# Optimization experiments

Hardware: AMD Instinct MI355X
Metric: run time of the kernel (lower is better)

The kernel has to match this reference:

```python
import jax, jax.numpy as jnp
import numpy as np

N_NODES = 20000
N_EDGES = 160000
N_GRAPHS = 64
IN_DIM = 128
HID = 512
N_ACT = 32


def gcn_conv(x, W, b, src, dst, n_nodes):
    # PyG GCNConv: add self-loops, symmetric normalization, x @ W then scatter-add.
    loop = jnp.arange(n_nodes, dtype=src.dtype)
    s = jnp.concatenate([src, loop])
    d = jnp.concatenate([dst, loop])
    deg = jax.ops.segment_sum(jnp.ones_like(d, dtype=x.dtype), d, num_segments=n_nodes)
    dinv = jnp.where(deg > 0, jax.lax.rsqrt(deg), 0.0)
    norm = dinv[s] * dinv[d]                      # [E+N]
    h = x @ W                                     # [N, out]
    msg = h[s] * norm[:, None]                    # gather + scale
    out = jax.ops.segment_sum(msg, d, num_segments=n_nodes)
    return out + b


def setup_inputs() -> dict:
    key = jax.random.key(0)
    ks = jax.random.split(key, 16)
    tree_x = jax.random.normal(ks[0], (N_NODES, IN_DIM), dtype=jnp.float32)
    edge_index = jax.random.randint(ks[1], (2, N_EDGES), 0, N_NODES, dtype=jnp.int32)
    # batch assignment: guarantee every graph id appears, then sort
    raw = jnp.concatenate([jnp.arange(N_GRAPHS, dtype=jnp.int32),
                           jax.random.randint(ks[2], (N_NODES - N_GRAPHS,), 0, N_GRAPHS, dtype=jnp.int32)])
    batch = jnp.sort(raw)

    def glorot(k, shape):
        lim = np.sqrt(6.0 / (shape[0] + shape[1]))
        return jax.random.uniform(k, shape, jnp.float32, -lim, lim)

    params = {
        'W1': glorot(ks[3], (IN_DIM, HID)), 'b1': jnp.zeros((HID,), jnp.float32),
        'W2': glorot(ks[4], (HID, HID)),    'b2': jnp.zeros((HID,), jnp.float32),
        'W3': glorot(ks[5], (HID, HID)),    'b3': jnp.zeros((HID,), jnp.float32),
        'Wf1': glorot(ks[6], (HID, HID)),   'bf1': jnp.zeros((HID,), jnp.float32),
        'Wf2': glorot(ks[7], (HID, HID)),   'bf2': jnp.zeros((HID,), jnp.float32),
        'Wf3': glorot(ks[8], (HID, HID)),   'bf3': jnp.zeros((HID,), jnp.float32),
        'Wo': glorot(ks[9], (HID, N_ACT)),  'bo': jnp.zeros((N_ACT,), jnp.float32),
    }
    return {'tree_x': tree_x, 'edge_index': edge_index, 'batch': batch, **params}


def reference(tree_x, edge_index, batch, W1, b1, W2, b2, W3, b3,
              Wf1, bf1, Wf2, bf2, Wf3, bf3, Wo, bo):
    src, dst = edge_index[0], edge_index[1]
    h = jax.nn.relu(gcn_conv(tree_x, W1, b1, src, dst, N_NODES))
    h = jax.nn.relu(gcn_conv(h, W2, b2, src, dst, N_NODES))
    h = jax.nn.relu(gcn_conv(h, W3, b3, src, dst, N_NODES))
    x = jax.ops.segment_max(h, batch, num_segments=N_GRAPHS)  # global_max_pool
    x = jax.nn.relu(x @ Wf1 + bf1)
    x = jax.nn.relu(x @ Wf2 + bf2)
    x = jax.nn.relu(x @ Wf3 + bf3)
    return x @ Wo + bo
```

## Files before the change

kernel.cpp:

```cpp
#include <hip/hip_runtime.h>
#include <stdint.h>

#define N_NODES 20000
#define N_EDGES 160000
#define N_GRAPHS 64
#define IN_DIM 128
#define HID 512
#define N_ACT 32

#define SCAN_NB ((N_NODES + 255) / 256)

typedef __attribute__((ext_vector_type(8))) short short8;
typedef __attribute__((ext_vector_type(4))) float f32x4;

__device__ __forceinline__ float bf2f(uint h16) {
    union { uint u; float f; } v; v.u = h16 << 16; return v.f;
}
__device__ __forceinline__ float bflo(uint u) {
    union { uint x; float f; } v; v.x = u << 16; return v.f;
}
__device__ __forceinline__ float bfhi(uint u) {
    union { uint x; float f; } v; v.x = u & 0xffff0000u; return v.f;
}
__device__ __forceinline__ ushort f2bf(float f) {
    union { float f; uint u; } v; v.f = f;
    uint u = v.u;
    uint r = (u + 0x7fffu + ((u >> 16) & 1u)) >> 16;
    return (ushort)r;
}

__device__ __forceinline__ void add8(float* acc, uint4 v) {
    acc[0] += bflo(v.x); acc[1] += bfhi(v.x);
    acc[2] += bflo(v.y); acc[3] += bfhi(v.y);
    acc[4] += bflo(v.z); acc[5] += bfhi(v.z);
    acc[6] += bflo(v.w); acc[7] += bfhi(v.w);
}


#define PB_HIST   625
#define PB_F2BF   (PB_HIST + 10000)
#define PB_WT1    (PB_F2BF + 64)
#define PB_WT2    (PB_WT1 + 256)
#define PB_WT3    (PB_WT2 + 256)
#define PB_BOUNDS (PB_WT3 + SCAN_NB)

__global__ __launch_bounds__(256) void k_prep(
    const int* __restrict__ edst, int* __restrict__ cnt,
    const float* __restrict__ tree_x, ushort* __restrict__ xbf,
    const float* __restrict__ W1, ushort* __restrict__ w1t,
    const float* __restrict__ W2, ushort* __restrict__ w2t,
    const float* __restrict__ W3, ushort* __restrict__ w3t,
    const int* __restrict__ batch, int* __restrict__ gstart)
{
    __shared__ float lds[32][33];
    int b = blockIdx.x;
    int t = threadIdx.x;
    int r = t >> 5, c = t & 31;
    if (b < PB_HIST) {
        int e = b * 256 + t;
        if (e < N_EDGES) atomicAdd(&cnt[edst[e]], 1);
    } else if (b < PB_F2BF) {
        int i = (b - PB_HIST) * 256 + t;
        if (i < N_NODES * IN_DIM) xbf[i] = f2bf(tree_x[i]);
    } else if (b < PB_WT1) {
        int tt = b - PB_F2BF;
        int kt = tt & 3, nt = tt >> 2;
        for (int rr = r; rr < 32; rr += 8)
            lds[rr][c] = W1[(size_t)(kt * 32 + rr) * HID + nt * 32 + c];
        __syncthreads();
        for (int rr = r; rr < 32; rr += 8)
            w1t[(size_t)(nt * 32 + rr) * IN_DIM + kt * 32 + c] = f2bf(lds[c][rr]);
    } else if (b < PB_WT2) {
        int tt = b - PB_WT1;
        int kt = tt & 15, nt = tt >> 4;
        for (int rr = r; rr < 32; rr += 8)
            lds[rr][c] = W2[(size_t)(kt * 32 + rr) * HID + nt * 32 + c];
        __syncthreads();
        for (int rr = r; rr < 32; rr += 8)
            w2t[(size_t)(nt * 32 + rr) * HID + kt * 32 + c] = f2bf(lds[c][rr]);
    } else if (b < PB_WT3) {
        int tt = b - PB_WT2;
        int kt = tt & 15, nt = tt >> 4;
        for (int rr = r; rr < 32; rr += 8)
            lds[rr][c] = W3[(size_t)(kt * 32 + rr) * HID + nt * 32 + c];
        __syncthreads();
        for (int rr = r; rr < 32; rr += 8)
            w3t[(size_t)(nt * 32 + rr) * HID + kt * 32 + c] = f2bf(lds[c][rr]);
    } else {
        int i = (b - PB_WT3) * 256 + t;
        if (i < N_NODES) {
            if (i == 0) {
                gstart[batch[0]] = 0;
                gstart[N_GRAPHS] = N_NODES;
            } else if (batch[i] != batch[i - 1]) {
                gstart[batch[i]] = i;
            }
        }
    }
}


__global__ __launch_bounds__(256) void k_part(const int* __restrict__ cnt, int* __restrict__ bsum) {
    __shared__ int s[256];
    int idx = blockIdx.x * 256 + threadIdx.x;
    s[threadIdx.x] = (idx < N_NODES) ? cnt[idx] : 0;
    __syncthreads();
    for (int off = 128; off > 0; off >>= 1) {
        if (threadIdx.x < off) s[threadIdx.x] += s[threadIdx.x + off];
        __syncthreads();
    }
    if (threadIdx.x == 0) bsum[blockIdx.x] = s[0];
}

__global__ __launch_bounds__(128) void k_scanb(const int* __restrict__ bsum,
                                               int* __restrict__ boff, int* __restrict__ rowstart) {
    __shared__ int s[128];
    int t = threadIdx.x;
    int own = (t < SCAN_NB) ? bsum[t] : 0;
    s[t] = own;
    __syncthreads();
    for (int off = 1; off < 128; off <<= 1) {
        int v = 0;
        if (t >= off) v = s[t - off];
        __syncthreads();
        s[t] += v;
        __syncthreads();
    }
    if (t < SCAN_NB) boff[t] = s[t] - own;
    if (t == SCAN_NB - 1) rowstart[N_NODES] = s[t];
}

__global__ __launch_bounds__(256) void k_final(
    const int* __restrict__ cnt, const int* __restrict__ boff,
    int* __restrict__ rowstart, int* __restrict__ cursor, float* __restrict__ dinv)
{
    __shared__ int s[256];
    int t = threadIdx.x;
    int idx = blockIdx.x * 256 + t;
    int c = (idx < N_NODES) ? cnt[idx] : 0;
    s[t] = c;
    __syncthreads();
    for (int off = 1; off < 256; off <<= 1) {
        int v = 0;
        if (t >= off) v = s[t - off];
        __syncthreads();
        s[t] += v;
        __syncthreads();
    }
    if (idx < N_NODES) {
        int start = boff[blockIdx.x] + s[t] - c;
        rowstart[idx] = start;
        cursor[idx] = start;
        dinv[idx] = rsqrtf((float)c + 1.0f);
    }
}

__global__ void k_fill(const int* __restrict__ src, const int* __restrict__ dst,
                       int* __restrict__ cursor, int* __restrict__ csr_src) {
    int e = blockIdx.x * 256 + threadIdx.x;
    if (e < N_EDGES) {
        int p = atomicAdd(&cursor[dst[e]], 1);
        csr_src[p] = src[e];
    }
}


__global__ __launch_bounds__(256) void k_gemm(
    const ushort* __restrict__ A, const ushort* __restrict__ Bt,
    const float* __restrict__ dinv, const float* __restrict__ bias,
    ushort* __restrict__ Out, int M, int Kdim, int mode)
{
    const int N = HID;
    __shared__ __align__(16) ushort lA[128 * 64];
    __shared__ __align__(16) ushort lB[128 * 64];
    int bm = blockIdx.x, bn = blockIdx.y;
    int tid = threadIdx.x;
    int wave = tid >> 6, lane = tid & 63;
    int wm = (wave >> 1) * 64, wn = (wave & 1) * 64;

    f32x4 acc[4][4] = {};

    int srow = lane >> 3;
    int scol = (lane & 7) * 8;

    for (int kt = 0; kt < Kdim; kt += 64) {
        for (int c = wave * 4; c < wave * 4 + 4; ++c) {
            int row = c * 8 + srow;
            int ga = bm * 128 + row; if (ga >= M) ga = M - 1;
            const ushort* gsA = A + (size_t)ga * Kdim + kt + scol;
            __builtin_amdgcn_global_load_lds(
                (const __attribute__((address_space(1))) void*)gsA,
                (__attribute__((address_space(3))) void*)(lA + c * 512), 16, 0, 0);
            int gb = bn * 128 + row;
            const ushort* gsB = Bt + (size_t)gb * Kdim + kt + scol;
            __builtin_amdgcn_global_load_lds(
                (const __attribute__((address_space(1))) void*)gsB,
                (__attribute__((address_space(3))) void*)(lB + c * 512), 16, 0, 0);
        }
        __syncthreads();
        for (int kk = 0; kk < 2; ++kk) {
            short8 af[4], bfr[4];
            int ko = kk * 32 + (lane >> 4) * 8;
            for (int m = 0; m < 4; ++m)
                af[m] = *(const short8*)&lA[(wm + m * 16 + (lane & 15)) * 64 + ko];
            for (int n = 0; n < 4; ++n)
                bfr[n] = *(const short8*)&lB[(wn + n * 16 + (lane & 15)) * 64 + ko];
            for (int m = 0; m < 4; ++m)
                for (int n = 0; n < 4; ++n)
                    acc[m][n] = __builtin_amdgcn_mfma_f32_16x16x32_bf16(af[m], bfr[n], acc[m][n], 0, 0, 0);
        }
        __syncthreads();
    }

    int cb = bn * 128 + wn + (lane & 15);
    float bb[4];
    if (mode == 1) {
        for (int n = 0; n < 4; ++n) bb[n] = bias[cb + n * 16];
    }
    for (int m = 0; m < 4; ++m) {
        int rbase = bm * 128 + wm + m * 16 + (lane >> 4) * 4;
        for (int j = 0; j < 4; ++j) {
            int r = rbase + j;
            if (r < M) {
                if (mode == 0) {
                    float dv = dinv[r];
                    for (int n = 0; n < 4; ++n)
                        Out[(size_t)r * N + cb + n * 16] = f2bf(acc[m][n][j] * dv);
                } else {
                    for (int n = 0; n < 4; ++n)
                        Out[(size_t)r * N + cb + n * 16] = f2bf(fmaxf(acc[m][n][j] + bb[n], 0.0f));
                }
            }
        }
    }
}


__global__ __launch_bounds__(256) void k_agg1(
    const ushort* __restrict__ Xin, const int* __restrict__ rowstart,
    const int* __restrict__ csr_src, const float* __restrict__ dinv,
    ushort* __restrict__ Y)
{
    int i = blockIdx.x * 4 + (threadIdx.x >> 6);
    if (i >= N_NODES) return;
    int lane = threadIdx.x & 63;
    const uint* xin = (const uint*)Xin;
    float dv = dinv[i];
    uint xi = xin[(size_t)i * 64 + lane];
    float a0 = dv * bflo(xi), a1 = dv * bfhi(xi);
    int e = rowstart[i], s1 = rowstart[i + 1];
    for (; e + 4 <= s1; e += 4) {
        int sa = csr_src[e], sb = csr_src[e + 1], sc = csr_src[e + 2], sd = csr_src[e + 3];
        float da = dinv[sa], db = dinv[sb], dc = dinv[sc], dd = dinv[sd];
        uint wa = xin[(size_t)sa * 64 + lane];
        uint wb = xin[(size_t)sb * 64 + lane];
        uint wc = xin[(size_t)sc * 64 + lane];
        uint wd = xin[(size_t)sd * 64 + lane];
        a0 = fmaf(da, bflo(wa), a0); a1 = fmaf(da, bfhi(wa), a1);
        a0 = fmaf(db, bflo(wb), a0); a1 = fmaf(db, bfhi(wb), a1);
        a0 = fmaf(dc, bflo(wc), a0); a1 = fmaf(dc, bfhi(wc), a1);
        a0 = fmaf(dd, bflo(wd), a0); a1 = fmaf(dd, bfhi(wd), a1);
    }
    for (; e < s1; ++e) {
        int sa = csr_src[e];
        float da = dinv[sa];
        uint wa = xin[(size_t)sa * 64 + lane];
        a0 = fmaf(da, bflo(wa), a0); a1 = fmaf(da, bfhi(wa), a1);
    }
    uint o = (uint)f2bf(dv * a0) | ((uint)f2bf(dv * a1) << 16);
    ((uint*)Y)[(size_t)i * 64 + lane] = o;
}


__global__ __launch_bounds__(256) void k_agg(
    const ushort* __restrict__ G, const int* __restrict__ rowstart,
    const int* __restrict__ csr_src, const float* __restrict__ dinv,
    const float* __restrict__ bias, ushort* __restrict__ X)
{
    int i = blockIdx.x * 4 + (threadIdx.x >> 6);
    if (i >= N_NODES) return;
    int lane = threadIdx.x & 63;
    const uint4* g4 = (const uint4*)G;

    uint4 a = g4[(size_t)i * 64 + lane];
    float acc[8] = { bflo(a.x), bfhi(a.x), bflo(a.y), bfhi(a.y),
                     bflo(a.z), bfhi(a.z), bflo(a.w), bfhi(a.w) };

    int e = rowstart[i], s1 = rowstart[i + 1];
    for (; e + 8 <= s1; e += 8) {
        int s0 = csr_src[e],     s1i = csr_src[e + 1], s2 = csr_src[e + 2], s3 = csr_src[e + 3];
        int s4 = csr_src[e + 4], s5 = csr_src[e + 5],  s6 = csr_src[e + 6], s7 = csr_src[e + 7];
        uint4 w0 = g4[(size_t)s0 * 64 + lane];
        uint4 w1 = g4[(size_t)s1i * 64 + lane];
        uint4 w2 = g4[(size_t)s2 * 64 + lane];
        uint4 w3 = g4[(size_t)s3 * 64 + lane];
        uint4 w4 = g4[(size_t)s4 * 64 + lane];
        uint4 w5 = g4[(size_t)s5 * 64 + lane];
        uint4 w6 = g4[(size_t)s6 * 64 + lane];
        uint4 w7 = g4[(size_t)s7 * 64 + lane];
        add8(acc, w0); add8(acc, w1); add8(acc, w2); add8(acc, w3);
        add8(acc, w4); add8(acc, w5); add8(acc, w6); add8(acc, w7);
    }
    for (; e + 4 <= s1; e += 4) {
        int s0 = csr_src[e], s1i = csr_src[e + 1], s2 = csr_src[e + 2], s3 = csr_src[e + 3];
        uint4 w0 = g4[(size_t)s0 * 64 + lane];
        uint4 w1 = g4[(size_t)s1i * 64 + lane];
        uint4 w2 = g4[(size_t)s2 * 64 + lane];
        uint4 w3 = g4[(size_t)s3 * 64 + lane];
        add8(acc, w0); add8(acc, w1); add8(acc, w2); add8(acc, w3);
    }
    for (; e < s1; ++e) {
        int s0 = csr_src[e];
        uint4 w0 = g4[(size_t)s0 * 64 + lane];
        add8(acc, w0);
    }

    float dv = dinv[i];
    float4 b0 = *(const float4*)(bias + lane * 8);
    float4 b1 = *(const float4*)(bias + lane * 8 + 4);
    float bb[8] = { b0.x, b0.y, b0.z, b0.w, b1.x, b1.y, b1.z, b1.w };

    uint4 o;
    uint p[8];
    for (int j = 0; j < 8; ++j)
        p[j] = f2bf(fmaxf(fmaf(dv, acc[j], bb[j]), 0.0f));
    o.x = p[0] | (p[1] << 16);
    o.y = p[2] | (p[3] << 16);
    o.z = p[4] | (p[5] << 16);
    o.w = p[6] | (p[7] << 16);
    *(uint4*)(X + (size_t)i * HID + lane * 8) = o;
}


__global__ __launch_bounds__(64) void k_pool(
    const ushort* __restrict__ X, const int* __restrict__ gstart, float* __restrict__ P)
{
    int g = blockIdx.x;
    int ch = blockIdx.y * 64 + threadIdx.x;
    float mx = -1e30f;
    int i0 = gstart[g], i1 = gstart[g + 1];
    int i = i0;
    for (; i + 4 <= i1; i += 4) {
        float a = bf2f(X[(size_t)(i + 0) * HID + ch]);
        float b = bf2f(X[(size_t)(i + 1) * HID + ch]);
        float c = bf2f(X[(size_t)(i + 2) * HID + ch]);
        float d = bf2f(X[(size_t)(i + 3) * HID + ch]);
        mx = fmaxf(mx, fmaxf(fmaxf(a, b), fmaxf(c, d)));
    }
    for (; i < i1; ++i) mx = fmaxf(mx, bf2f(X[(size_t)i * HID + ch]));
    P[(size_t)g * HID + ch] = mx;
}


__global__ __launch_bounds__(256) void k_fc(
    const float* __restrict__ in, const float* __restrict__ W,
    const float* __restrict__ b, float* __restrict__ out,
    int K, int NO, int relu)
{
    __shared__ float xs[HID];
    __shared__ float part[4][64];
    int g = blockIdx.x;
    int j0 = blockIdx.y * 64;
    int tid = threadIdx.x;
    int wave = tid >> 6, lane = tid & 63;

    for (int k = tid; k < K; k += 256) xs[k] = in[(size_t)g * K + k];
    __syncthreads();

    int j = j0 + lane;
    bool active = (j < NO);
    int kpw = K >> 2;
    int k0 = wave * kpw;
    float acc = 0.0f;
    if (active) {
        const float* wp = W + (size_t)k0 * NO + j;
        int k = 0;
        for (; k + 4 <= kpw; k += 4) {
            float w0 = wp[(size_t)(k + 0) * NO];
            float w1 = wp[(size_t)(k + 1) * NO];
            float w2 = wp[(size_t)(k + 2) * NO];
            float w3 = wp[(size_t)(k + 3) * NO];
            acc = fmaf(xs[k0 + k + 0], w0, acc);
            acc = fmaf(xs[k0 + k + 1], w1, acc);
            acc = fmaf(xs[k0 + k + 2], w2, acc);
            acc = fmaf(xs[k0 + k + 3], w3, acc);
        }
        for (; k < kpw; ++k)
            acc = fmaf(xs[k0 + k], wp[(size_t)k * NO], acc);
    }
    part[wave][lane] = acc;
    __syncthreads();
    if (wave == 0 && active) {
        float a = part[0][lane] + part[1][lane] + part[2][lane] + part[3][lane] + b[j];
        if (relu) a = fmaxf(a, 0.0f);
        out[(size_t)g * NO + j] = a;
    }
}


extern "C" void kernel_launch(void* const* d_in, const int* in_sizes, int n_in,
                              void* d_out, int out_size, void* d_ws, size_t ws_size,
                              hipStream_t stream) {
    const float* tree_x = (const float*)d_in[0];
    const int*   ei     = (const int*)d_in[1];
    const int*   batch  = (const int*)d_in[2];
    const float* W1  = (const float*)d_in[3];  const float* b1  = (const float*)d_in[4];
    const float* W2  = (const float*)d_in[5];  const float* b2  = (const float*)d_in[6];
    const float* W3  = (const float*)d_in[7];  const float* b3  = (const float*)d_in[8];
    const float* Wf1 = (const float*)d_in[9];  const float* bf1 = (const float*)d_in[10];
    const float* Wf2 = (const float*)d_in[11]; const float* bf2 = (const float*)d_in[12];
    const float* Wf3 = (const float*)d_in[13]; const float* bf3 = (const float*)d_in[14];
    const float* Wo  = (const float*)d_in[15]; const float* bo  = (const float*)d_in[16];

    char* w = (char*)d_ws;
    size_t off = 0;
    auto alloc = [&](size_t bytes) -> void* {
        void* p = w + off;
        off += (bytes + 255) & ~(size_t)255;
        return p;
    };
    int*    cnt      = (int*)alloc((size_t)N_NODES * 4);
    int*    cursor   = (int*)alloc((size_t)N_NODES * 4);
    int*    rowstart = (int*)alloc((size_t)(N_NODES + 1) * 4);
    float*  dinv     = (float*)alloc((size_t)N_NODES * 4);
    int*    csr      = (int*)alloc((size_t)N_EDGES * 4);
    int*    gstart   = (int*)alloc((size_t)(N_GRAPHS + 1) * 4);
    int*    bsum     = (int*)alloc((size_t)SCAN_NB * 4);
    int*    boff     = (int*)alloc((size_t)SCAN_NB * 4);
    ushort* xbf      = (ushort*)alloc((size_t)N_NODES * IN_DIM * 2);
    ushort* ybuf     = (ushort*)alloc((size_t)N_NODES * IN_DIM * 2);
    ushort* w1t      = (ushort*)alloc((size_t)HID * IN_DIM * 2);
    ushort* w2t      = (ushort*)alloc((size_t)HID * HID * 2);
    ushort* w3t      = (ushort*)alloc((size_t)HID * HID * 2);
    ushort* gbuf     = (ushort*)alloc((size_t)N_NODES * HID * 2);
    ushort* xbuf     = (ushort*)alloc((size_t)N_NODES * HID * 2);
    float*  P0       = (float*)alloc((size_t)N_GRAPHS * HID * 4);
    float*  P1       = (float*)alloc((size_t)N_GRAPHS * HID * 4);

    const int* esrc = ei;
    const int* edst = ei + N_EDGES;

    hipMemsetAsync(cnt, 0, (size_t)N_NODES * 4, stream);
    k_prep<<<PB_BOUNDS, 256, 0, stream>>>(edst, cnt, tree_x, xbf,
                                          W1, w1t, W2, w2t, W3, w3t, batch, gstart);
    k_part<<<SCAN_NB, 256, 0, stream>>>(cnt, bsum);
    k_scanb<<<1, 128, 0, stream>>>(bsum, boff, rowstart);
    k_final<<<SCAN_NB, 256, 0, stream>>>(cnt, boff, rowstart, cursor, dinv);
    k_fill<<<(N_EDGES + 255) / 256, 256, 0, stream>>>(esrc, edst, cursor, csr);

    dim3 gemm_grid((N_NODES + 127) / 128, HID / 128);

    k_agg1<<<N_NODES / 4, 256, 0, stream>>>(xbf, rowstart, csr, dinv, ybuf);
    k_gemm<<<gemm_grid, 256, 0, stream>>>(ybuf, w1t, dinv, b1, xbuf, N_NODES, IN_DIM, 1);
    k_gemm<<<gemm_grid, 256, 0, stream>>>(xbuf, w2t, dinv, b2, gbuf, N_NODES, HID, 0);
    k_agg<<<N_NODES / 4, 256, 0, stream>>>(gbuf, rowstart, csr, dinv, b2, xbuf);
    k_gemm<<<gemm_grid, 256, 0, stream>>>(xbuf, w3t, dinv, b3, gbuf, N_NODES, HID, 0);
    k_agg<<<N_NODES / 4, 256, 0, stream>>>(gbuf, rowstart, csr, dinv, b3, xbuf);

    k_pool<<<dim3(N_GRAPHS, 8), 64, 0, stream>>>(xbuf, gstart, P0);

    k_fc<<<dim3(N_GRAPHS, HID / 64), 256, 0, stream>>>(P0, Wf1, bf1, P1, HID, HID, 1);
    k_fc<<<dim3(N_GRAPHS, HID / 64), 256, 0, stream>>>(P1, Wf2, bf2, P0, HID, HID, 1);
    k_fc<<<dim3(N_GRAPHS, HID / 64), 256, 0, stream>>>(P0, Wf3, bf3, P1, HID, HID, 1);
    k_fc<<<dim3(N_GRAPHS, 1), 256, 0, stream>>>(P1, Wo, bo, (float*)d_out, HID, N_ACT, 0);
}
```

Before: 240.3 us.

## Split aggregation across column groups with edge-parallel half-waves

The aggregation kernel for layers 2 and 3 is restructured. Each wave used to handle one node across all 512 channels with 16-byte gathers. Now a 2D grid splits the channels into 8 column groups of 64, and the two half-waves each take alternate edges and combine their partial sums with a cross-lane shuffle. This raises parallelism and memory-level concurrency per node, but the gathers shrink to 4 bytes, only 128 bytes are contiguous per neighbour row, and the index loads are repeated for every column group.

```diff
diff --git a/kernel.cpp b/kernel.cpp
--- a/kernel.cpp
+++ b/kernel.cpp
@@ -27,13 +27,6 @@
     uint u = v.u;
     uint r = (u + 0x7fffu + ((u >> 16) & 1u)) >> 16;
     return (ushort)r;
-}
-
-__device__ __forceinline__ void add8(float* acc, uint4 v) {
-    acc[0] += bflo(v.x); acc[1] += bfhi(v.x);
-    acc[2] += bflo(v.y); acc[3] += bfhi(v.y);
-    acc[4] += bflo(v.z); acc[5] += bfhi(v.z);
-    acc[6] += bflo(v.w); acc[7] += bfhi(v.w);
 }
 
 
@@ -272,63 +265,48 @@
 }
 
 
-__global__ __launch_bounds__(256) void k_agg(
+__global__ __launch_bounds__(256) void k_agg_cs(
     const ushort* __restrict__ G, const int* __restrict__ rowstart,
     const int* __restrict__ csr_src, const float* __restrict__ dinv,
     const float* __restrict__ bias, ushort* __restrict__ X)
 {
     int i = blockIdx.x * 4 + (threadIdx.x >> 6);
-    if (i >= N_NODES) return;
     int lane = threadIdx.x & 63;
-    const uint4* g4 = (const uint4*)G;
-
-    uint4 a = g4[(size_t)i * 64 + lane];
-    float acc[8] = { bflo(a.x), bfhi(a.x), bflo(a.y), bfhi(a.y),
-                     bflo(a.z), bfhi(a.z), bflo(a.w), bfhi(a.w) };
-
-    int e = rowstart[i], s1 = rowstart[i + 1];
-    for (; e + 8 <= s1; e += 8) {
-        int s0 = csr_src[e],     s1i = csr_src[e + 1], s2 = csr_src[e + 2], s3 = csr_src[e + 3];
-        int s4 = csr_src[e + 4], s5 = csr_src[e + 5],  s6 = csr_src[e + 6], s7 = csr_src[e + 7];
-        uint4 w0 = g4[(size_t)s0 * 64 + lane];
-        uint4 w1 = g4[(size_t)s1i * 64 + lane];
-        uint4 w2 = g4[(size_t)s2 * 64 + lane];
-        uint4 w3 = g4[(size_t)s3 * 64 + lane];
-        uint4 w4 = g4[(size_t)s4 * 64 + lane];
-        uint4 w5 = g4[(size_t)s5 * 64 + lane];
-        uint4 w6 = g4[(size_t)s6 * 64 + lane];
-        uint4 w7 = g4[(size_t)s7 * 64 + lane];
-        add8(acc, w0); add8(acc, w1); add8(acc, w2); add8(acc, w3);
-        add8(acc, w4); add8(acc, w5); add8(acc, w6); add8(acc, w7);
-    }
-    for (; e + 4 <= s1; e += 4) {
-        int s0 = csr_src[e], s1i = csr_src[e + 1], s2 = csr_src[e + 2], s3 = csr_src[e + 3];
-        uint4 w0 = g4[(size_t)s0 * 64 + lane];
-        uint4 w1 = g4[(size_t)s1i * 64 + lane];
-        uint4 w2 = g4[(size_t)s2 * 64 + lane];
-        uint4 w3 = g4[(size_t)s3 * 64 + lane];
-        add8(acc, w0); add8(acc, w1); add8(acc, w2); add8(acc, w3);
-    }
-    for (; e < s1; ++e) {
-        int s0 = csr_src[e];
-        uint4 w0 = g4[(size_t)s0 * 64 + lane];
-        add8(acc, w0);
-    }
-
-    float dv = dinv[i];
-    float4 b0 = *(const float4*)(bias + lane * 8);
-    float4 b1 = *(const float4*)(bias + lane * 8 + 4);
-    float bb[8] = { b0.x, b0.y, b0.z, b0.w, b1.x, b1.y, b1.z, b1.w };
-
-    uint4 o;
-    uint p[8];
-    for (int j = 0; j < 8; ++j)
-        p[j] = f2bf(fmaxf(fmaf(dv, acc[j], bb[j]), 0.0f));
-    o.x = p[0] | (p[1] << 16);
-    o.y = p[2] | (p[3] << 16);
-    o.z = p[4] | (p[5] << 16);
-    o.w = p[6] | (p[7] << 16);
-    *(uint4*)(X + (size_t)i * HID + lane * 8) = o;
+    int half = lane >> 5;
+    int cl = lane & 31;
+    int cg = blockIdx.y;
+    const uint* gu = (const uint*)G;
+    size_t colbase = (size_t)cg * 32 + cl;
+
+    uint sv = gu[(size_t)i * 256 + colbase];
+    float a0 = half ? 0.0f : bflo(sv);
+    float a1 = half ? 0.0f : bfhi(sv);
+
+    int e0 = rowstart[i], e1 = rowstart[i + 1];
+    int e = e0 + half;
+    for (; e + 4 <= e1; e += 4) {
+        int sa = csr_src[e], sb = csr_src[e + 2];
+        uint va = gu[(size_t)sa * 256 + colbase];
+        uint vb = gu[(size_t)sb * 256 + colbase];
+        a0 += bflo(va); a1 += bfhi(va);
+        a0 += bflo(vb); a1 += bfhi(vb);
+    }
+    for (; e < e1; e += 2) {
+        int sa = csr_src[e];
+        uint va = gu[(size_t)sa * 256 + colbase];
+        a0 += bflo(va); a1 += bfhi(va);
+    }
+
+    a0 += __shfl_xor(a0, 32);
+    a1 += __shfl_xor(a1, 32);
+
+    if (half == 0) {
+        float dv = dinv[i];
+        float2 bb = ((const float2*)bias)[colbase];
+        uint o = (uint)f2bf(fmaxf(fmaf(dv, a0, bb.x), 0.0f))
+               | ((uint)f2bf(fmaxf(fmaf(dv, a1, bb.y), 0.0f)) << 16);
+        ((uint*)X)[(size_t)i * 256 + colbase] = o;
+    }
 }
 
 
@@ -449,13 +427,14 @@
     k_fill<<<(N_EDGES + 255) / 256, 256, 0, stream>>>(esrc, edst, cursor, csr);
 
     dim3 gemm_grid((N_NODES + 127) / 128, HID / 128);
+    dim3 agg_grid(N_NODES / 4, 8);
 
     k_agg1<<<N_NODES / 4, 256, 0, stream>>>(xbf, rowstart, csr, dinv, ybuf);
     k_gemm<<<gemm_grid, 256, 0, stream>>>(ybuf, w1t, dinv, b1, xbuf, N_NODES, IN_DIM, 1);
     k_gemm<<<gemm_grid, 256, 0, stream>>>(xbuf, w2t, dinv, b2, gbuf, N_NODES, HID, 0);
-    k_agg<<<N_NODES / 4, 256, 0, stream>>>(gbuf, rowstart, csr, dinv, b2, xbuf);
+    k_agg_cs<<<agg_grid, 256, 0, stream>>>(gbuf, rowstart, csr, dinv, b2, xbuf);
     k_gemm<<<gemm_grid, 256, 0, stream>>>(xbuf, w3t, dinv, b3, gbuf, N_NODES, HID, 0);
-    k_agg<<<N_NODES / 4, 256, 0, stream>>>(gbuf, rowstart, csr, dinv, b3, xbuf);
+    k_agg_cs<<<agg_grid, 256, 0, stream>>>(gbuf, rowstart, csr, dinv, b3, xbuf);
 
     k_pool<<<dim3(N_GRAPHS, 8), 64, 0, stream>>>(xbuf, gstart, P0);
 
```

Result: slower. 317.0 us (+31.9%).
